# Kernel tuning notes

Measured on AMD Instinct MI355X. Metric: run time of the kernel, lower is better.

Reference implementation:

```python
import jax, jax.numpy as jnp
import numpy as np

HEADS = 16
D_HID = 64
N_EMBED = HEADS * D_HID  # 1024; also must equal k_len for the final out @ v


def setup_inputs() -> dict:
    key = jax.random.key(0)
    kq, kk, kv, km = jax.random.split(key, 4)
    B, QL, KL = 4, 2048, 1024
    q = jax.random.normal(kq, (B, QL, N_EMBED), dtype=jnp.float32)
    k = jax.random.normal(kk, (B, KL, N_EMBED), dtype=jnp.float32)
    v = jax.random.normal(kv, (B, KL, N_EMBED), dtype=jnp.float32)
    mask = jax.random.randint(km, (B, QL, 1, KL), 0, 2, dtype=jnp.int32)
    return {"q": q, "k": k, "v": v, "mask": mask}


def reference(q, k, v, mask):
    B, QL, E = q.shape
    KL = k.shape[1]
    H, D = HEADS, D_HID
    qh = q.reshape(B, QL, H, D)
    kh = k.reshape(B, KL, H, D)
    vh = v.reshape(B, KL, H, D)
    # energy: (B, q, h, k), softmax over key axis (dim=3 in the original)
    energy = jnp.einsum('nqhd,nkhd->nqhk', qh, kh)
    energy = jnp.where(mask == 0, jnp.float32(-1e20), energy)
    attention = jax.nn.softmax(energy / jnp.sqrt(jnp.float32(E)), axis=3)
    out = jnp.einsum('nqhk,nkhd->nqhd', attention, vh).reshape(B, QL, H * D)
    # second softmax over the model dim (self.softmax = nn.Softmax(dim=-1))
    out = jax.nn.softmax(out, axis=-1)
    # out @ v : (B, QL, E) @ (B, KL==E, E) -> (B, QL, E)
    v2 = jnp.matmul(out, v)
    return (v2, out)
```

## Files before the change

### kernel.cpp

```cpp
#include <hip/hip_runtime.h>
#include <hip/hip_bf16.h>
#include <stdint.h>

#define HEADS 16
#define DH 64
#define NE 1024
#define BB 4
#define QL 2048
#define KLEN 1024

typedef __attribute__((ext_vector_type(8))) short bf16x8;
typedef __attribute__((ext_vector_type(4))) float f32x4;
typedef unsigned short u16;
typedef unsigned int u32;
typedef unsigned long long u64;

__device__ __forceinline__ u16 f2b(float f){
  union { float f; unsigned u; } v; v.f = f;
  unsigned r = v.u + 0x7fffu + ((v.u >> 16) & 1u);
  return (u16)(r >> 16);
}
__device__ __forceinline__ u32 pack2(float a, float b){
  return (u32)f2b(a) | ((u32)f2b(b) << 16);
}
__device__ __forceinline__ u32 cvtpk(float a, float b){
  u32 r; asm("v_cvt_pk_bf16_f32 %0, %1, %2" : "=v"(r) : "v"(a), "v"(b)); return r;
}
__device__ __forceinline__ void gload16(const void* g, void* l){
  __builtin_amdgcn_global_load_lds((const __attribute__((address_space(1))) u32*)g,
                                   (__attribute__((address_space(3))) u32*)l, 16, 0, 0);
}

__global__ __launch_bounds__(256) void kpack_kernel(const float* __restrict__ k,
    u16* __restrict__ kp){
  int id = blockIdx.x * 256 + threadIdx.x;
  int u = id & 511, kt = (id >> 9) & 15, h = (id >> 13) & 15, b = id >> 17;
  int row = u >> 3, blk = u & 7, d0 = ((blk ^ (row & 7)) << 3);
  const float* src = k + ((size_t)(b * KLEN + kt * 64 + row)) * NE + h * DH + d0;
  float4 f0 = *(const float4*)src;
  float4 f1 = *(const float4*)(src + 4);
  uint4 o;
  o.x = pack2(f0.x, f0.y); o.y = pack2(f0.z, f0.w);
  o.z = pack2(f1.x, f1.y); o.w = pack2(f1.z, f1.w);
  ((uint4*)kp)[id] = o;
}

__global__ __launch_bounds__(256) void vpack_kernel(const float* __restrict__ v,
    u16* __restrict__ vp){
  __shared__ __attribute__((aligned(16))) u16 t[64][72];
  const int b = blockIdx.z, h = blockIdx.y, kt = blockIdx.x;
  const int tid = threadIdx.x;
  {
    int key = tid >> 2, dseg = (tid & 3) * 16;
    const float* src = v + ((size_t)(b * KLEN + kt * 64 + key)) * NE + h * DH + dseg;
#pragma unroll
    for (int i = 0; i < 16; i += 4){
      float4 f = *(const float4*)(src + i);
      t[dseg + i + 0][key] = f2b(f.x); t[dseg + i + 1][key] = f2b(f.y);
      t[dseg + i + 2][key] = f2b(f.z); t[dseg + i + 3][key] = f2b(f.w);
    }
  }
  __syncthreads();
  {
    int row = tid >> 2, p2 = (tid & 3) * 2;
    u16* dst = vp + ((size_t)((b * HEADS + h) * 16 + kt)) * 4096;
#pragma unroll
    for (int e = 0; e < 2; e++){
      int blk = p2 + e, sb = blk ^ (row & 7);
      uint4 d4 = *(const uint4*)&t[row][sb * 8];
      *(uint4*)(dst + (row * 8 + blk) * 8) = d4;
    }
  }
}

__global__ __launch_bounds__(256) void mbits_kernel(const int* __restrict__ mask,
    u64* __restrict__ mb){
  int t = blockIdx.x * 256 + threadIdx.x;
  u64 bal = __ballot(mask[t] != 0);
  if ((threadIdx.x & 63) == 0) mb[t >> 6] = bal;
}

__global__ __launch_bounds__(256) void attn1_kernel(
    const float* __restrict__ q, const u16* __restrict__ kp,
    const u16* __restrict__ vp, const u64* __restrict__ mb,
    float* __restrict__ out1){
  __shared__ __attribute__((aligned(16))) u16 Kt[2][4096];
  __shared__ __attribute__((aligned(16))) u16 Vt[2][4096];
  __shared__ u64 LUT[16];
  const int b = blockIdx.z, h = blockIdx.y, q0 = blockIdx.x * 128;
  const int tid = threadIdx.x, w = tid >> 6, l = tid & 63;
  const int lq = l & 15, g = l >> 4;
  const int qrowA = q0 + w * 32 + lq;
  const int qrowB = qrowA + 16;
  const float C2 = 0.0450842200278f;

  if (tid < 16){
    u32 n = tid;
    u32 m0 = (n & 1 ? 0xFFFFu : 0u) | (n & 2 ? 0xFFFF0000u : 0u);
    u32 m1 = (n & 4 ? 0xFFFFu : 0u) | (n & 8 ? 0xFFFF0000u : 0u);
    LUT[n] = (u64)m0 | ((u64)m1 << 32);
  }

  bf16x8 bqA0, bqA1, bqB0, bqB1;
#define LOADQ(D0, D1, QROW) {                                                  \
    const float* qsrc = q + ((size_t)b * QL + (QROW)) * NE + h * DH + g * 8;   \
    float4 f0 = *(const float4*)(qsrc);                                        \
    float4 f1 = *(const float4*)(qsrc + 4);                                    \
    float4 f2 = *(const float4*)(qsrc + 32);                                   \
    float4 f3 = *(const float4*)(qsrc + 36);                                   \
    D0[0]=(short)f2b(f0.x*C2); D0[1]=(short)f2b(f0.y*C2);                      \
    D0[2]=(short)f2b(f0.z*C2); D0[3]=(short)f2b(f0.w*C2);                      \
    D0[4]=(short)f2b(f1.x*C2); D0[5]=(short)f2b(f1.y*C2);                      \
    D0[6]=(short)f2b(f1.z*C2); D0[7]=(short)f2b(f1.w*C2);                      \
    D1[0]=(short)f2b(f2.x*C2); D1[1]=(short)f2b(f2.y*C2);                      \
    D1[2]=(short)f2b(f2.z*C2); D1[3]=(short)f2b(f2.w*C2);                      \
    D1[4]=(short)f2b(f3.x*C2); D1[5]=(short)f2b(f3.y*C2);                      \
    D1[6]=(short)f2b(f3.z*C2); D1[7]=(short)f2b(f3.w*C2); }
  LOADQ(bqA0, bqA1, qrowA)
  LOADQ(bqB0, bqB1, qrowB)
#undef LOADQ

  const f32x4 fz = {0.f, 0.f, 0.f, 0.f};
  f32x4 accOA[4], accOB[4];
#pragma unroll
  for (int t2 = 0; t2 < 4; t2++){ accOA[t2] = fz; accOB[t2] = fz; }
  f32x4 accLA = fz, accLB = fz;
  const short one_bf = (short)0x3F80;
  const bf16x8 ones = {one_bf, one_bf, one_bf, one_bf, one_bf, one_bf, one_bf, one_bf};

  const u64* mrowA = mb + ((size_t)b * QL + qrowA) * (KLEN / 64);
  const u64* mrowB = mb + ((size_t)b * QL + qrowB) * (KLEN / 64);
  const u16* kT0 = kp + ((size_t)((b * HEADS + h) * 16)) * 4096;
  const u16* vT0 = vp + ((size_t)((b * HEADS + h) * 16)) * 4096;
  const int blkA = g ^ (lq & 7);
  const int bK0 = lq * 128 + blkA * 16;
  const int bK1 = lq * 128 + (blkA ^ 4) * 16;
  char* KtC = (char*)Kt;
  char* VtC = (char*)Vt;

  gload16(kT0 + (size_t)tid * 8,         KtC + w * 1024);
  gload16(kT0 + (size_t)(256 + tid) * 8, KtC + 4096 + w * 1024);
  gload16(vT0 + (size_t)tid * 8,         VtC + w * 1024);
  gload16(vT0 + (size_t)(256 + tid) * 8, VtC + 4096 + w * 1024);

  int cur = 0;
  for (int kt = 0; kt < 16; ++kt){
    __syncthreads();
    if (kt < 15){
      const u16* ksn = kT0 + (size_t)(kt + 1) * 4096;
      const u16* vsn = vT0 + (size_t)(kt + 1) * 4096;
      char* Kd = KtC + (cur ^ 1) * 8192;
      char* Vd = VtC + (cur ^ 1) * 8192;
      gload16(ksn + (size_t)tid * 8,         Kd + w * 1024);
      gload16(ksn + (size_t)(256 + tid) * 8, Kd + 4096 + w * 1024);
      gload16(vsn + (size_t)tid * 8,         Vd + w * 1024);
      gload16(vsn + (size_t)(256 + tid) * 8, Vd + 4096 + w * 1024);
    }
    u64 mwA = mrowA[kt], mwB = mrowB[kt];
    const char* Kb = KtC + cur * 8192;
    const char* Vb = VtC + cur * 8192;

    f32x4 sA[4], sB[4];
#pragma unroll
    for (int c = 0; c < 4; c++){ sA[c] = fz; sB[c] = fz; }
#pragma unroll
    for (int c = 0; c < 4; c++){
      bf16x8 a0 = *(const bf16x8*)(Kb + bK0 + c * 2048);
      bf16x8 a1 = *(const bf16x8*)(Kb + bK1 + c * 2048);
      sA[c] = __builtin_amdgcn_mfma_f32_16x16x32_bf16(a0, bqA0, sA[c], 0, 0, 0);
      sA[c] = __builtin_amdgcn_mfma_f32_16x16x32_bf16(a1, bqA1, sA[c], 0, 0, 0);
      sB[c] = __builtin_amdgcn_mfma_f32_16x16x32_bf16(a0, bqB0, sB[c], 0, 0, 0);
      sB[c] = __builtin_amdgcn_mfma_f32_16x16x32_bf16(a1, bqB1, sB[c], 0, 0, 0);
    }

#define SOFTMAX_SUB(SV, MW, PB0, PB1, ACCL)                                    \
    {                                                                          \
      u32 pw[8];                                                               \
      _Pragma("unroll") for (int c = 0; c < 4; c++){                           \
        float p0 = __builtin_amdgcn_exp2f(SV[c][0]);                           \
        float p1 = __builtin_amdgcn_exp2f(SV[c][1]);                           \
        float p2 = __builtin_amdgcn_exp2f(SV[c][2]);                           \
        float p3 = __builtin_amdgcn_exp2f(SV[c][3]);                           \
        pw[2 * c]     = cvtpk(p0, p1);                                         \
        pw[2 * c + 1] = cvtpk(p2, p3);                                         \
      }                                                                        \
      {                                                                        \
        u32 mwlo = (u32)(MW), mwhi = (u32)((MW) >> 32);                        \
        int s0_ = 4 * g;                                                       \
        u64 M0 = LUT[(mwlo >> s0_) & 0xFu];                                    \
        u64 M1 = LUT[(mwlo >> (s0_ + 16)) & 0xFu];                             \
        u64 M2 = LUT[(mwhi >> s0_) & 0xFu];                                    \
        u64 M3 = LUT[(mwhi >> (s0_ + 16)) & 0xFu];                             \
        pw[0] &= (u32)M0; pw[1] &= (u32)(M0 >> 32);                            \
        pw[2] &= (u32)M1; pw[3] &= (u32)(M1 >> 32);                            \
        pw[4] &= (u32)M2; pw[5] &= (u32)(M2 >> 32);                            \
        pw[6] &= (u32)M3; pw[7] &= (u32)(M3 >> 32);                            \
      }                                                                        \
      PB0.u4.x = pw[0]; PB0.u4.y = pw[1]; PB0.u4.z = pw[2]; PB0.u4.w = pw[3];  \
      PB1.u4.x = pw[4]; PB1.u4.y = pw[5]; PB1.u4.z = pw[6]; PB1.u4.w = pw[7];  \
      ACCL = __builtin_amdgcn_mfma_f32_16x16x32_bf16(ones, PB0.v8, ACCL, 0, 0, 0);\
      ACCL = __builtin_amdgcn_mfma_f32_16x16x32_bf16(ones, PB1.v8, ACCL, 0, 0, 0);\
    }

    union bfu { uint4 u4; bf16x8 v8; };
    bfu pbA0, pbA1, pbB0, pbB1;
    SOFTMAX_SUB(sA, mwA, pbA0, pbA1, accLA)
    SOFTMAX_SUB(sB, mwB, pbB0, pbB1, accLB)
#undef SOFTMAX_SUB

    {
      const int gOff = (g & 1) * 8;
      const int gHi = g >> 1;
#pragma unroll
      for (int t2 = 0; t2 < 4; t2++){
        const char* vrow = Vb + (t2 * 16 + lq) * 128;
        const int rx = lq & 7;
        bfu va0, va1;
        {
          uint2 lo_ = *(const uint2*)(vrow + (((0 + gHi) ^ rx) << 4) + gOff);
          uint2 hi_ = *(const uint2*)(vrow + (((2 + gHi) ^ rx) << 4) + gOff);
          va0.u4.x = lo_.x; va0.u4.y = lo_.y; va0.u4.z = hi_.x; va0.u4.w = hi_.y;
        }
        {
          uint2 lo_ = *(const uint2*)(vrow + (((4 + gHi) ^ rx) << 4) + gOff);
          uint2 hi_ = *(const uint2*)(vrow + (((6 + gHi) ^ rx) << 4) + gOff);
          va1.u4.x = lo_.x; va1.u4.y = lo_.y; va1.u4.z = hi_.x; va1.u4.w = hi_.y;
        }
        accOA[t2] = __builtin_amdgcn_mfma_f32_16x16x32_bf16(va0.v8, pbA0.v8, accOA[t2], 0, 0, 0);
        accOA[t2] = __builtin_amdgcn_mfma_f32_16x16x32_bf16(va1.v8, pbA1.v8, accOA[t2], 0, 0, 0);
        accOB[t2] = __builtin_amdgcn_mfma_f32_16x16x32_bf16(va0.v8, pbB0.v8, accOB[t2], 0, 0, 0);
        accOB[t2] = __builtin_amdgcn_mfma_f32_16x16x32_bf16(va1.v8, pbB1.v8, accOB[t2], 0, 0, 0);
      }
    }
    cur ^= 1;
  }

  float liA = 1.f / accLA[0];
  float liB = 1.f / accLB[0];
  float* opA = out1 + ((size_t)b * QL + qrowA) * NE + h * DH + 4 * g;
  float* opB = out1 + ((size_t)b * QL + qrowB) * NE + h * DH + 4 * g;
#pragma unroll
  for (int t2 = 0; t2 < 4; t2++){
    float4 stA = {accOA[t2][0] * liA, accOA[t2][1] * liA,
                  accOA[t2][2] * liA, accOA[t2][3] * liA};
    float4 stB = {accOB[t2][0] * liB, accOB[t2][1] * liB,
                  accOB[t2][2] * liB, accOB[t2][3] * liB};
    *(float4*)(opA + t2 * 16) = stA;
    *(float4*)(opB + t2 * 16) = stB;
  }
}

__global__ __launch_bounds__(256) void softmax2_kernel(float* __restrict__ o,
    u16* __restrict__ wp){
  const int row = blockIdx.x, tid = threadIdx.x;
  float* p = o + (size_t)row * NE + tid * 4;
  float4 x = *(const float4*)p;
  float mx = fmaxf(fmaxf(x.x, x.y), fmaxf(x.z, x.w));
#pragma unroll
  for (int off = 32; off >= 1; off >>= 1) mx = fmaxf(mx, __shfl_xor(mx, off, 64));
  __shared__ float red[8];
  const int wv = tid >> 6;
  if ((tid & 63) == 0) red[wv] = mx;
  __syncthreads();
  mx = fmaxf(fmaxf(red[0], red[1]), fmaxf(red[2], red[3]));
  float e0 = __expf(x.x - mx), e1 = __expf(x.y - mx);
  float e2 = __expf(x.z - mx), e3 = __expf(x.w - mx);
  float s = (e0 + e1) + (e2 + e3);
#pragma unroll
  for (int off = 32; off >= 1; off >>= 1) s += __shfl_xor(s, off, 64);
  if ((tid & 63) == 0) red[4 + wv] = s;
  __syncthreads();
  s = (red[4] + red[5]) + (red[6] + red[7]);
  float inv = 1.f / s;
  x.x = e0 * inv; x.y = e1 * inv; x.z = e2 * inv; x.w = e3 * inv;
  *(float4*)p = x;
  if (wp){
    int b = row >> 11, qi = row & 2047;
    int qt = qi >> 6, rw = qi & 63;
    int ktile = tid >> 4, db = (tid >> 1) & 7, half = tid & 1;
    size_t tile = (size_t)((b * 32 + qt) * 16 + ktile);
    char* dst = (char*)wp + tile * 8192 + rw * 128 + ((db ^ (rw & 7)) * 16) + half * 8;
    uint2 u2; u2.x = cvtpk(x.x, x.y); u2.y = cvtpk(x.z, x.w);
    *(uint2*)dst = u2;
  }
}

__global__ __launch_bounds__(256) void gemm3f_kernel(const u16* __restrict__ wp,
    const u16* __restrict__ vp, float* __restrict__ v2){
  __shared__ __attribute__((aligned(16))) u16 Wt[2][4096];
  __shared__ __attribute__((aligned(16))) u16 Vt3[2][4096];
  const int b = blockIdx.z, qt = blockIdx.y, h3 = blockIdx.x;
  const int tid = threadIdx.x, w = tid >> 6, l = tid & 63;
  const int lq = l & 15, g = l >> 4;
  const int blkA = g ^ (lq & 7);
  const int bK0 = lq * 128 + blkA * 16;
  const int bK1 = lq * 128 + (blkA ^ 4) * 16;
  char* WtC = (char*)Wt;
  char* VtC = (char*)Vt3;
  const f32x4 fz = {0.f, 0.f, 0.f, 0.f};
  f32x4 acc[4];
#pragma unroll
  for (int t2 = 0; t2 < 4; t2++) acc[t2] = fz;
  const u16* wT0 = wp + ((size_t)((b * 32 + qt) * 16)) * 4096;
  const u16* vT0 = vp + ((size_t)((b * HEADS + h3) * 16)) * 4096;

  gload16(wT0 + (size_t)tid * 8,         WtC + w * 1024);
  gload16(wT0 + (size_t)(256 + tid) * 8, WtC + 4096 + w * 1024);
  gload16(vT0 + (size_t)tid * 8,         VtC + w * 1024);
  gload16(vT0 + (size_t)(256 + tid) * 8, VtC + 4096 + w * 1024);

  int cur = 0;
  for (int ksv = 0; ksv < 16; ++ksv){
    __syncthreads();
    if (ksv < 15){
      const u16* wsn = wT0 + (size_t)(ksv + 1) * 4096;
      const u16* vsn = vT0 + (size_t)(ksv + 1) * 4096;
      char* Wd = WtC + (cur ^ 1) * 8192;
      char* Vd = VtC + (cur ^ 1) * 8192;
      gload16(wsn + (size_t)tid * 8,         Wd + w * 1024);
      gload16(wsn + (size_t)(256 + tid) * 8, Wd + 4096 + w * 1024);
      gload16(vsn + (size_t)tid * 8,         Vd + w * 1024);
      gload16(vsn + (size_t)(256 + tid) * 8, Vd + 4096 + w * 1024);
    }
    const char* Wb = WtC + cur * 8192;
    const char* Vb = VtC + cur * 8192;
    bf16x8 a0 = *(const bf16x8*)(Wb + w * 2048 + bK0);
    bf16x8 a1 = *(const bf16x8*)(Wb + w * 2048 + bK1);
#pragma unroll
    for (int t2 = 0; t2 < 4; t2++){
      bf16x8 b0 = *(const bf16x8*)(Vb + bK0 + t2 * 2048);
      bf16x8 b1 = *(const bf16x8*)(Vb + bK1 + t2 * 2048);
      acc[t2] = __builtin_amdgcn_mfma_f32_16x16x32_bf16(a0, b0, acc[t2], 0, 0, 0);
      acc[t2] = __builtin_amdgcn_mfma_f32_16x16x32_bf16(a1, b1, acc[t2], 0, 0, 0);
    }
    cur ^= 1;
  }
  float* op = v2 + ((size_t)b * QL + qt * 64 + w * 16) * NE + h3 * 64;
#pragma unroll
  for (int t2 = 0; t2 < 4; t2++){
#pragma unroll
    for (int r = 0; r < 4; r++){
      op[(4 * g + r) * NE + t2 * 16 + lq] = acc[t2][r];
    }
  }
}

__global__ __launch_bounds__(256) void gemm3_kernel(const float* __restrict__ w2,
    const u16* __restrict__ vp, float* __restrict__ v2){
  __shared__ __attribute__((aligned(16))) u16 Wt[4096];
  __shared__ __attribute__((aligned(16))) u16 Vt3[4096];
  const int b = blockIdx.z, q0 = blockIdx.y * 64, n0 = blockIdx.x * 64;
  const int tid = threadIdx.x, w = tid >> 6, l = tid & 63;
  const int lq = l & 15, g = l >> 4;
  const int blkA = g ^ (lq & 7);
  const int bK0 = lq * 128 + blkA * 16;
  const int bK1 = lq * 128 + (blkA ^ 4) * 16;
  char* WtC = (char*)Wt;
  char* VtC = (char*)Vt3;
  const f32x4 fz = {0.f, 0.f, 0.f, 0.f};
  f32x4 acc[4];
#pragma unroll
  for (int t2 = 0; t2 < 4; t2++) acc[t2] = fz;
  const float* wsrc0 = w2 + ((size_t)b * QL + q0) * NE;
  const u16* vT0 = vp + ((size_t)((b * HEADS + (n0 >> 6)) * 16)) * 4096;
  const int rr = tid >> 4, cc = tid & 15;

  for (int ksv = 0; ksv < 16; ++ksv){
    __syncthreads();
#pragma unroll
    for (int pp = 0; pp < 4; pp++){
      int r2 = pp * 16 + rr;
      float4 f = *(const float4*)(wsrc0 + (size_t)r2 * NE + ksv * 64 + cc * 4);
      int blkL = (cc >> 1) ^ (r2 & 7);
      uint2 u2; u2.x = cvtpk(f.x, f.y); u2.y = cvtpk(f.z, f.w);
      *(uint2*)(WtC + (r2 * 8 + blkL) * 16 + (cc & 1) * 8) = u2;
    }
    const u16* vs = vT0 + ksv * 4096;
    gload16(vs + (size_t)tid * 8,         VtC + w * 1024);
    gload16(vs + (size_t)(256 + tid) * 8, VtC + 4096 + w * 1024);
    __syncthreads();
    bf16x8 a0 = *(const bf16x8*)(WtC + w * 2048 + bK0);
    bf16x8 a1 = *(const bf16x8*)(WtC + w * 2048 + bK1);
#pragma unroll
    for (int t2 = 0; t2 < 4; t2++){
      bf16x8 b0 = *(const bf16x8*)(VtC + bK0 + t2 * 2048);
      bf16x8 b1 = *(const bf16x8*)(VtC + bK1 + t2 * 2048);
      acc[t2] = __builtin_amdgcn_mfma_f32_16x16x32_bf16(a0, b0, acc[t2], 0, 0, 0);
      acc[t2] = __builtin_amdgcn_mfma_f32_16x16x32_bf16(a1, b1, acc[t2], 0, 0, 0);
    }
  }
  float* op = v2 + ((size_t)b * QL + q0 + w * 16) * NE + n0;
#pragma unroll
  for (int t2 = 0; t2 < 4; t2++){
#pragma unroll
    for (int r = 0; r < 4; r++){
      op[(4 * g + r) * NE + t2 * 16 + lq] = acc[t2][r];
    }
  }
}

extern "C" void kernel_launch(void* const* d_in, const int* in_sizes, int n_in,
                              void* d_out, int out_size, void* d_ws, size_t ws_size,
                              hipStream_t stream){
  const float* q = (const float*)d_in[0];
  const float* k = (const float*)d_in[1];
  const float* v = (const float*)d_in[2];
  const int* mask = (const int*)d_in[3];
  float* v2 = (float*)d_out;
  float* out2 = v2 + (size_t)BB * QL * NE;

  char* wsb = (char*)d_ws;
  u16* kp  = (u16*)wsb;
  u16* vpk = (u16*)(wsb + (8u << 20));
  u64* mbp = (u64*)(wsb + (16u << 20));
  u16* wpk = (u16*)(wsb + (17u << 20));
  const bool fast = ws_size >= (34ull << 20);

  kpack_kernel<<<2048, 256, 0, stream>>>(k, kp);
  vpack_kernel<<<dim3(16, HEADS, BB), 256, 0, stream>>>(v, vpk);
  mbits_kernel<<<BB * QL * KLEN / 256, 256, 0, stream>>>(mask, mbp);
  attn1_kernel<<<dim3(QL / 128, HEADS, BB), 256, 0, stream>>>(q, kp, vpk, mbp, out2);
  softmax2_kernel<<<BB * QL, 256, 0, stream>>>(out2, fast ? wpk : (u16*)nullptr);
  if (fast){
    gemm3f_kernel<<<dim3(NE / 64, QL / 64, BB), 256, 0, stream>>>(wpk, vpk, v2);
  } else {
    gemm3_kernel<<<dim3(NE / 64, QL / 64, BB), 256, 0, stream>>>(out2, vpk, v2);
  }
}
```

Before: 142.8 us.

## Prepack scaled bf16 Q and swizzle block order in attention and GEMM

Adds a qpack kernel that scales Q and converts it to bf16 in workspace, so attn1 loads half the bytes for Q and skips the per-block conversion when the workspace is large enough. It also flattens the attn1 and gemm3f grids into 1D and remaps block indices so that groups of 8 consecutive blocks share the same K/V (or W) tiles, aiming for better L2 reuse. The cost is an extra kernel launch plus a full extra read and write of Q. The Q path only runs when the workspace is at least 49 MB.

```diff
diff --git a/kernel.cpp b/kernel.cpp
--- a/kernel.cpp
+++ b/kernel.cpp
@@ -45,6 +45,19 @@
   ((uint4*)kp)[id] = o;
 }
 
+__global__ __launch_bounds__(256) void qpack_kernel(const float* __restrict__ q,
+    u16* __restrict__ qp){
+  const float C2 = 0.0450842200278f;
+  int i = blockIdx.x * 256 + threadIdx.x;
+  const float* s = q + (size_t)i * 8;
+  float4 f0 = *(const float4*)s;
+  float4 f1 = *(const float4*)(s + 4);
+  uint4 o;
+  o.x = pack2(f0.x * C2, f0.y * C2); o.y = pack2(f0.z * C2, f0.w * C2);
+  o.z = pack2(f1.x * C2, f1.y * C2); o.w = pack2(f1.z * C2, f1.w * C2);
+  ((uint4*)qp)[i] = o;
+}
+
 __global__ __launch_bounds__(256) void vpack_kernel(const float* __restrict__ v,
     u16* __restrict__ vp){
   __shared__ __attribute__((aligned(16))) u16 t[64][72];
@@ -83,11 +96,15 @@
 __global__ __launch_bounds__(256) void attn1_kernel(
     const float* __restrict__ q, const u16* __restrict__ kp,
     const u16* __restrict__ vp, const u64* __restrict__ mb,
-    float* __restrict__ out1){
+    const u16* __restrict__ qp, float* __restrict__ out1){
   __shared__ __attribute__((aligned(16))) u16 Kt[2][4096];
   __shared__ __attribute__((aligned(16))) u16 Vt[2][4096];
   __shared__ u64 LUT[16];
-  const int b = blockIdx.z, h = blockIdx.y, q0 = blockIdx.x * 128;
+  const int D = blockIdx.x;
+  const int qt = (D >> 3) & 15;
+  const int grp = (D & 7) + 8 * (D >> 7);
+  const int h = grp & 15, b = grp >> 4;
+  const int q0 = qt * 128;
   const int tid = threadIdx.x, w = tid >> 6, l = tid & 63;
   const int lq = l & 15, g = l >> 4;
   const int qrowA = q0 + w * 32 + lq;
@@ -102,6 +119,14 @@
   }
 
   bf16x8 bqA0, bqA1, bqB0, bqB1;
+  if (qp){
+    const u16* qsA = qp + ((size_t)b * QL + qrowA) * NE + h * DH + g * 8;
+    const u16* qsB = qp + ((size_t)b * QL + qrowB) * NE + h * DH + g * 8;
+    bqA0 = *(const bf16x8*)(qsA);
+    bqA1 = *(const bf16x8*)(qsA + 32);
+    bqB0 = *(const bf16x8*)(qsB);
+    bqB1 = *(const bf16x8*)(qsB + 32);
+  } else {
 #define LOADQ(D0, D1, QROW) {                                                  \
     const float* qsrc = q + ((size_t)b * QL + (QROW)) * NE + h * DH + g * 8;   \
     float4 f0 = *(const float4*)(qsrc);                                        \
@@ -116,9 +141,10 @@
     D1[2]=(short)f2b(f2.z*C2); D1[3]=(short)f2b(f2.w*C2);                      \
     D1[4]=(short)f2b(f3.x*C2); D1[5]=(short)f2b(f3.y*C2);                      \
     D1[6]=(short)f2b(f3.z*C2); D1[7]=(short)f2b(f3.w*C2); }
-  LOADQ(bqA0, bqA1, qrowA)
-  LOADQ(bqB0, bqB1, qrowB)
+    LOADQ(bqA0, bqA1, qrowA)
+    LOADQ(bqB0, bqB1, qrowB)
 #undef LOADQ
+  }
 
   const f32x4 fz = {0.f, 0.f, 0.f, 0.f};
   f32x4 accOA[4], accOB[4];
@@ -289,7 +315,10 @@
     const u16* __restrict__ vp, float* __restrict__ v2){
   __shared__ __attribute__((aligned(16))) u16 Wt[2][4096];
   __shared__ __attribute__((aligned(16))) u16 Vt3[2][4096];
-  const int b = blockIdx.z, qt = blockIdx.y, h3 = blockIdx.x;
+  const int D = blockIdx.x;
+  const int h3 = (D >> 3) & 15;
+  const int grp = (D & 7) + 8 * (D >> 7);
+  const int qt = grp & 31, b = grp >> 5;
   const int tid = threadIdx.x, w = tid >> 6, l = tid & 63;
   const int lq = l & 15, g = l >> 4;
   const int blkA = g ^ (lq & 7);
@@ -414,15 +443,18 @@
   u16* vpk = (u16*)(wsb + (8u << 20));
   u64* mbp = (u64*)(wsb + (16u << 20));
   u16* wpk = (u16*)(wsb + (17u << 20));
+  u16* qpp = (u16*)(wsb + (33u << 20));
   const bool fast = ws_size >= (34ull << 20);
+  const bool useQ = ws_size >= (49ull << 20);
 
   kpack_kernel<<<2048, 256, 0, stream>>>(k, kp);
   vpack_kernel<<<dim3(16, HEADS, BB), 256, 0, stream>>>(v, vpk);
   mbits_kernel<<<BB * QL * KLEN / 256, 256, 0, stream>>>(mask, mbp);
-  attn1_kernel<<<dim3(QL / 128, HEADS, BB), 256, 0, stream>>>(q, kp, vpk, mbp, out2);
+  if (useQ) qpack_kernel<<<4096, 256, 0, stream>>>(q, qpp);
+  attn1_kernel<<<1024, 256, 0, stream>>>(q, kp, vpk, mbp, useQ ? qpp : (u16*)nullptr, out2);
   softmax2_kernel<<<BB * QL, 256, 0, stream>>>(out2, fast ? wpk : (u16*)nullptr);
   if (fast){
-    gemm3f_kernel<<<dim3(NE / 64, QL / 64, BB), 256, 0, stream>>>(wpk, vpk, v2);
+    gemm3f_kernel<<<2048, 256, 0, stream>>>(wpk, vpk, v2);
   } else {
     gemm3_kernel<<<dim3(NE / 64, QL / 64, BB), 256, 0, stream>>>(out2, vpk, v2);
   }
```

Result: no change. 144.8 us (+1.4%).
